# Kernel tuning notes

Measured on AMD Instinct MI355X. Metric: run time of the kernel, lower is better.

The kernel has to match this reference:

```python
import jax, jax.numpy as jnp
import numpy as np

ALPHA = 20.0 / 100.0  # dt / tau
NOISE_SCALE = 0.1 * (2.0 * ALPHA) ** 0.5  # network_noise * sqrt(2*alpha)

T, B, I, H, O = 512, 64, 128, 512, 64


def setup_inputs() -> dict:
    key = jax.random.key(0)
    ks = jax.random.split(key, 6)
    s_in = 1.0 / np.sqrt(I)
    s_h = 1.0 / np.sqrt(H)
    return {
        "x": jax.random.normal(ks[0], (T, B, I), jnp.float32),
        "noise": jax.random.normal(ks[1], (T, B, H), jnp.float32),
        "W_in": jax.random.normal(ks[2], (H, I), jnp.float32) * s_in,
        "W_rec": jax.random.normal(ks[3], (H, H), jnp.float32) * s_h,
        "b_rec": jnp.zeros((H,), jnp.float32),
        "W_out": jax.random.normal(ks[4], (O, H), jnp.float32) * s_h,
        "b_out": jnp.zeros((O,), jnp.float32),
    }


def reference(x, noise, W_in, W_rec, b_rec, W_out, b_out):
    # Precompute input projection for all timesteps: (T, B, H)
    xin = jnp.einsum("tbi,hi->tbh", x, W_in)

    def step(hidden, inp):
        xin_t, noise_t = inp
        h_new = jax.nn.relu(xin_t + hidden @ W_rec.T + b_rec)
        h_new = hidden * (1.0 - ALPHA) + h_new * ALPHA
        h_new = h_new + noise_t * NOISE_SCALE
        return h_new, h_new

    h0 = jnp.zeros((x.shape[1], W_rec.shape[0]), x.dtype)
    _, rnn_output = jax.lax.scan(step, h0, (xin, noise))  # (T, B, H)
    output = jnp.einsum("tbh,oh->tbo", rnn_output, W_out) + b_out
    return output, rnn_output
```

## Files before the change

kernel.cpp:

```cpp
#include <hip/hip_runtime.h>

constexpr int T  = 512;
constexpr int NB = 64;
constexpr int NI = 128;
constexpr int NH = 512;
constexpr int NO = 64;

constexpr float ALPHA = 0.2f;
constexpr float NSC   = 0.063245553203367586f;

typedef _Float16 h2_t __attribute__((ext_vector_type(2)));

#if defined(__has_builtin)
#  if __has_builtin(__builtin_amdgcn_fdot2)
#    define HAS_FDOT2 1
#  endif
#endif
#ifndef HAS_FDOT2
#  define HAS_FDOT2 0
#endif

__device__ __forceinline__ float dot2(uint32_t wbits, uint32_t hbits, float acc) {
#if HAS_FDOT2
    return __builtin_amdgcn_fdot2(__builtin_bit_cast(h2_t, wbits),
                                  __builtin_bit_cast(h2_t, hbits), acc, false);
#else
    const h2_t wv = __builtin_bit_cast(h2_t, wbits);
    const h2_t hv = __builtin_bit_cast(h2_t, hbits);
    return acc + (float)wv.x * (float)hv.x + (float)wv.y * (float)hv.y;
#endif
}

__global__ __launch_bounds__(256) void k_gemm_nt_bias(
    const float* __restrict__ A, const float* __restrict__ Bm,
    const float* __restrict__ bias, float* __restrict__ C,
    int M, int N, int K)
{
    __shared__ __align__(16) float As[32][68];
    __shared__ __align__(16) float Bs[32][68];
    const int tid = threadIdx.x;
    const int tx = tid & 15, ty = tid >> 4;
    const long row0 = (long)blockIdx.x * 64;
    const long col0 = (long)blockIdx.y * 64;
    const int lr = tid >> 3;
    const int lq = tid & 7;

    float acc[4][4] = {};

    for (int kt = 0; kt < K; kt += 32) {
        #pragma unroll
        for (int hh = 0; hh < 2; ++hh) {
            const int r = lr + hh * 32;
            const float4 va = *(const float4*)&A[(size_t)(row0 + r) * K + kt + lq * 4];
            As[lq*4+0][r] = va.x; As[lq*4+1][r] = va.y;
            As[lq*4+2][r] = va.z; As[lq*4+3][r] = va.w;
            const float4 vb = *(const float4*)&Bm[(size_t)(col0 + r) * K + kt + lq * 4];
            Bs[lq*4+0][r] = vb.x; Bs[lq*4+1][r] = vb.y;
            Bs[lq*4+2][r] = vb.z; Bs[lq*4+3][r] = vb.w;
        }
        __syncthreads();
        #pragma unroll
        for (int kk = 0; kk < 32; ++kk) {
            const float4 a4 = *(const float4*)&As[kk][ty * 4];
            const float4 b4 = *(const float4*)&Bs[kk][tx * 4];
            const float a[4] = {a4.x, a4.y, a4.z, a4.w};
            const float b[4] = {b4.x, b4.y, b4.z, b4.w};
            #pragma unroll
            for (int i = 0; i < 4; ++i)
                #pragma unroll
                for (int j = 0; j < 4; ++j)
                    acc[i][j] += a[i] * b[j];
        }
        __syncthreads();
    }

    #pragma unroll
    for (int i = 0; i < 4; ++i) {
        const long r = row0 + ty * 4 + i;
        const int  cc = (int)col0 + tx * 4;
        float4 ov;
        ov.x = acc[i][0] + bias[cc + 0];
        ov.y = acc[i][1] + bias[cc + 1];
        ov.z = acc[i][2] + bias[cc + 2];
        ov.w = acc[i][3] + bias[cc + 3];
        *(float4*)&C[(size_t)r * N + cc] = ov;
    }
}

__device__ __forceinline__ uint32_t pack_h(float h, uint32_t tag) {
    const _Float16 hf = (_Float16)h;
    const uint32_t hb = __builtin_bit_cast(unsigned short, hf);
    return (hb << 16) | (tag & 0xFFFFu);
}

__global__ __launch_bounds__(512, 2) void k_rnn(
    const float* __restrict__ W_rec,
    const float* __restrict__ noise,
    float* __restrict__ rnn,
    uint32_t* __restrict__ ex)
{
    const int bid = blockIdx.x;
    const int g = bid & 63;
    const int m = bid >> 6;
    const int tid = threadIdx.x;
    const int w = tid >> 6;
    const int l = tid & 63;

    __shared__ __align__(16) unsigned short hbf[NH];
    __shared__ __align__(16) float pr[8][128];

    uint32_t wp0[32], wp1[32];
    {
        const float* p0 = W_rec + (size_t)(m * 128 + l) * NH + w * 64;
        const float* p1 = W_rec + (size_t)(m * 128 + l + 64) * NH + w * 64;
        #pragma unroll
        for (int i = 0; i < 16; ++i) {
            const float4 a = *(const float4*)(p0 + i * 4);
            uint32_t u0 = __builtin_bit_cast(uint32_t,
                (h2_t){(_Float16)a.x, (_Float16)a.y});
            uint32_t u1 = __builtin_bit_cast(uint32_t,
                (h2_t){(_Float16)a.z, (_Float16)a.w});
            asm volatile("" : "+v"(u0), "+v"(u1));
            wp0[i * 2] = u0; wp0[i * 2 + 1] = u1;
            const float4 b = *(const float4*)(p1 + i * 4);
            uint32_t v0 = __builtin_bit_cast(uint32_t,
                (h2_t){(_Float16)b.x, (_Float16)b.y});
            uint32_t v1 = __builtin_bit_cast(uint32_t,
                (h2_t){(_Float16)b.z, (_Float16)b.w});
            asm volatile("" : "+v"(v0), "+v"(v1));
            wp1[i * 2] = v0; wp1[i * 2 + 1] = v1;
        }
    }

    const int gc = m * 128 + tid;

    const int q    = tid - 128;
    const int pp   = q >> 7;
    const int pm   = pp + (pp >= m ? 1 : 0);
    const int pcol = pm * 128 + (q & 127);

    hbf[tid] = 0;

    float hreg = 0.f;

    float xin_pf = 0.f, noi_pf = 0.f;
    if (tid < 128) {
        xin_pf = rnn[(size_t)g * NH + gc];
        noi_pf = noise[(size_t)g * NH + gc];
    }
    __syncthreads();

    int alive  = 1;
    int budget = 1 << 16;

    for (int t = 0; t < T; ++t) {
        float aA0 = 0.f, aA1 = 0.f, aB0 = 0.f, aB1 = 0.f;
        {
            const uint4* hp = (const uint4*)&hbf[w * 64];
            #pragma unroll
            for (int i = 0; i < 8; ++i) {
                const uint4 u = hp[i];
                aA0 = dot2(wp0[i*4+0], u.x, aA0);
                aA1 = dot2(wp0[i*4+1], u.y, aA1);
                aA0 = dot2(wp0[i*4+2], u.z, aA0);
                aA1 = dot2(wp0[i*4+3], u.w, aA1);
                aB0 = dot2(wp1[i*4+0], u.x, aB0);
                aB1 = dot2(wp1[i*4+1], u.y, aB1);
                aB0 = dot2(wp1[i*4+2], u.z, aB0);
                aB1 = dot2(wp1[i*4+3], u.w, aB1);
            }
        }
        pr[w][l]      = aA0 + aA1;
        pr[w][l + 64] = aB0 + aB1;
        __syncthreads();

        const uint32_t want = (uint32_t)(t + 1);
        uint32_t* slot = ex + (size_t)(t & 1) * NB * NH;

        if (tid < 128) {
            float sum = 0.f;
            #pragma unroll
            for (int k = 0; k < 8; ++k) sum += pr[k][tid];
            const float hn = fmaxf(xin_pf + sum, 0.f);
            const float nw = (1.f - ALPHA) * hreg + ALPHA * hn + NSC * noi_pf;
            hreg = nw;
            const uint32_t pk = pack_h(nw, want);
            (void)__hip_atomic_exchange(&slot[(size_t)g * NH + gc], pk,
                                        __ATOMIC_RELAXED, __HIP_MEMORY_SCOPE_AGENT);
            hbf[gc] = (unsigned short)(pk >> 16);
            rnn[((size_t)t * NB + g) * NH + gc] = nw;
            const int tn = (t + 1 < T) ? (t + 1) : t;
            xin_pf = rnn[((size_t)tn * NB + g) * NH + gc];
            noi_pf = noise[((size_t)tn * NB + g) * NH + gc];
        } else {
            uint32_t v;
            if (alive) {
                for (;;) {
                    v = __hip_atomic_fetch_or(&slot[(size_t)g * NH + pcol], 0u,
                                              __ATOMIC_RELAXED, __HIP_MEMORY_SCOPE_AGENT);
                    if ((v & 0xFFFFu) == (want & 0xFFFFu)) break;
                    __builtin_amdgcn_s_sleep(1);
                    if (--budget < 0) { alive = 0; break; }
                }
            } else {
                v = __hip_atomic_fetch_or(&slot[(size_t)g * NH + pcol], 0u,
                                          __ATOMIC_RELAXED, __HIP_MEMORY_SCOPE_AGENT);
            }
            hbf[pcol] = (unsigned short)(v >> 16);
        }
        __syncthreads();
    }
}

extern "C" void kernel_launch(void* const* d_in, const int* in_sizes, int n_in,
                              void* d_out, int out_size, void* d_ws, size_t ws_size,
                              hipStream_t stream)
{
    (void)in_sizes; (void)n_in; (void)out_size; (void)ws_size;
    const float* x     = (const float*)d_in[0];
    const float* noise = (const float*)d_in[1];
    const float* W_in  = (const float*)d_in[2];
    const float* W_rec = (const float*)d_in[3];
    const float* b_rec = (const float*)d_in[4];
    const float* W_out = (const float*)d_in[5];
    const float* b_out = (const float*)d_in[6];

    float* out = (float*)d_out;
    float* rnn = out + (size_t)T * NB * NO;

    uint32_t* ex = (uint32_t*)d_ws;

    hipMemsetAsync(ex, 0, (size_t)2 * NB * NH * sizeof(uint32_t), stream);

    hipLaunchKernelGGL(k_gemm_nt_bias, dim3((T * NB) / 64, NH / 64), dim3(256), 0, stream,
                       x, W_in, b_rec, rnn, T * NB, NH, NI);

    hipLaunchKernelGGL(k_rnn, dim3(256), dim3(512), 0, stream,
                       W_rec, noise, rnn, ex);

    hipLaunchKernelGGL(k_gemm_nt_bias, dim3((T * NB) / 64, NO / 64), dim3(256), 0, stream,
                       rnn, W_out, b_out, out, T * NB, NO, NH);
}
```

Before: 732.9 us.

## Stage fp16 recurrent weights in swizzled LDS instead of registers

Each block now converts its 128-row slice of W_rec to fp16 once and stores it in about 128 KB of dynamic shared memory with an XOR swizzle, instead of holding 64 packed weights per thread in VGPRs. Every timestep re-reads the weights from LDS with 16-byte loads alongside the hidden-state reads. The launch-bounds occupancy hint is dropped and the large dynamic LDS size is set explicitly, which limits the CU to one block. The aim is to cut register pressure, but it adds LDS traffic to every serial recurrence step.

```diff
diff --git a/kernel.cpp b/kernel.cpp
--- a/kernel.cpp
+++ b/kernel.cpp
@@ -29,6 +29,10 @@
     const h2_t hv = __builtin_bit_cast(h2_t, hbits);
     return acc + (float)wv.x * (float)hv.x + (float)wv.y * (float)hv.y;
 #endif
+}
+
+__device__ __forceinline__ uint32_t pk2(float x, float y) {
+    return __builtin_bit_cast(uint32_t, (h2_t){(_Float16)x, (_Float16)y});
 }
 
 __global__ __launch_bounds__(256) void k_gemm_nt_bias(
@@ -93,12 +97,17 @@
     return (hb << 16) | (tag & 0xFFFFu);
 }
 
-__global__ __launch_bounds__(512, 2) void k_rnn(
+__global__ __launch_bounds__(512) void k_rnn(
     const float* __restrict__ W_rec,
     const float* __restrict__ noise,
     float* __restrict__ rnn,
     uint32_t* __restrict__ ex)
 {
+    extern __shared__ __align__(16) char smem[];
+    unsigned short* Wl  = (unsigned short*)smem;
+    unsigned short* hbf = (unsigned short*)(smem + 131072);
+    float*          pr  = (float*)(smem + 132096);
+
     const int bid = blockIdx.x;
     const int g = bid & 63;
     const int m = bid >> 6;
@@ -106,29 +115,26 @@
     const int w = tid >> 6;
     const int l = tid & 63;
 
-    __shared__ __align__(16) unsigned short hbf[NH];
-    __shared__ __align__(16) float pr[8][128];
-
-    uint32_t wp0[32], wp1[32];
     {
         const float* p0 = W_rec + (size_t)(m * 128 + l) * NH + w * 64;
         const float* p1 = W_rec + (size_t)(m * 128 + l + 64) * NH + w * 64;
+        const int s = (l & 7) << 4;
+        char* b0 = (char*)Wl + l * 1024 + w * 128 + s;
+        char* b1 = b0 + 65536;
         #pragma unroll
-        for (int i = 0; i < 16; ++i) {
-            const float4 a = *(const float4*)(p0 + i * 4);
-            uint32_t u0 = __builtin_bit_cast(uint32_t,
-                (h2_t){(_Float16)a.x, (_Float16)a.y});
-            uint32_t u1 = __builtin_bit_cast(uint32_t,
-                (h2_t){(_Float16)a.z, (_Float16)a.w});
-            asm volatile("" : "+v"(u0), "+v"(u1));
-            wp0[i * 2] = u0; wp0[i * 2 + 1] = u1;
-            const float4 b = *(const float4*)(p1 + i * 4);
-            uint32_t v0 = __builtin_bit_cast(uint32_t,
-                (h2_t){(_Float16)b.x, (_Float16)b.y});
-            uint32_t v1 = __builtin_bit_cast(uint32_t,
-                (h2_t){(_Float16)b.z, (_Float16)b.w});
-            asm volatile("" : "+v"(v0), "+v"(v1));
-            wp1[i * 2] = v0; wp1[i * 2 + 1] = v1;
+        for (int j = 0; j < 8; ++j) {
+            const float4 qa0 = *(const float4*)(p0 + j * 8);
+            const float4 qa1 = *(const float4*)(p0 + j * 8 + 4);
+            uint4 ca;
+            ca.x = pk2(qa0.x, qa0.y); ca.y = pk2(qa0.z, qa0.w);
+            ca.z = pk2(qa1.x, qa1.y); ca.w = pk2(qa1.z, qa1.w);
+            *(uint4*)((uintptr_t)b0 ^ (unsigned)(j << 4)) = ca;
+            const float4 qb0 = *(const float4*)(p1 + j * 8);
+            const float4 qb1 = *(const float4*)(p1 + j * 8 + 4);
+            uint4 cb;
+            cb.x = pk2(qb0.x, qb0.y); cb.y = pk2(qb0.z, qb0.w);
+            cb.z = pk2(qb1.x, qb1.y); cb.w = pk2(qb1.z, qb1.w);
+            *(uint4*)((uintptr_t)b1 ^ (unsigned)(j << 4)) = cb;
         }
     }
 
@@ -152,26 +158,27 @@
 
     int alive  = 1;
     int budget = 1 << 16;
+
+    const char* wb0 = (const char*)Wl + l * 1024 + w * 128 + ((l & 7) << 4);
+    const char* wb1 = wb0 + 65536;
 
     for (int t = 0; t < T; ++t) {
         float aA0 = 0.f, aA1 = 0.f, aB0 = 0.f, aB1 = 0.f;
         {
             const uint4* hp = (const uint4*)&hbf[w * 64];
             #pragma unroll
-            for (int i = 0; i < 8; ++i) {
-                const uint4 u = hp[i];
-                aA0 = dot2(wp0[i*4+0], u.x, aA0);
-                aA1 = dot2(wp0[i*4+1], u.y, aA1);
-                aA0 = dot2(wp0[i*4+2], u.z, aA0);
-                aA1 = dot2(wp0[i*4+3], u.w, aA1);
-                aB0 = dot2(wp1[i*4+0], u.x, aB0);
-                aB1 = dot2(wp1[i*4+1], u.y, aB1);
-                aB0 = dot2(wp1[i*4+2], u.z, aB0);
-                aB1 = dot2(wp1[i*4+3], u.w, aB1);
+            for (int j = 0; j < 8; ++j) {
+                const uint4 u = hp[j];
+                const uint4 A = *(const uint4*)((uintptr_t)wb0 ^ (unsigned)(j << 4));
+                const uint4 B = *(const uint4*)((uintptr_t)wb1 ^ (unsigned)(j << 4));
+                aA0 = dot2(A.x, u.x, aA0); aA1 = dot2(A.y, u.y, aA1);
+                aA0 = dot2(A.z, u.z, aA0); aA1 = dot2(A.w, u.w, aA1);
+                aB0 = dot2(B.x, u.x, aB0); aB1 = dot2(B.y, u.y, aB1);
+                aB0 = dot2(B.z, u.z, aB0); aB1 = dot2(B.w, u.w, aB1);
             }
         }
-        pr[w][l]      = aA0 + aA1;
-        pr[w][l + 64] = aB0 + aB1;
+        pr[w * 128 + l]      = aA0 + aA1;
+        pr[w * 128 + l + 64] = aB0 + aB1;
         __syncthreads();
 
         const uint32_t want = (uint32_t)(t + 1);
@@ -180,7 +187,7 @@
         if (tid < 128) {
             float sum = 0.f;
             #pragma unroll
-            for (int k = 0; k < 8; ++k) sum += pr[k][tid];
+            for (int k = 0; k < 8; ++k) sum += pr[k * 128 + tid];
             const float hn = fmaxf(xin_pf + sum, 0.f);
             const float nw = (1.f - ALPHA) * hreg + ALPHA * hn + NSC * noi_pf;
             hreg = nw;
@@ -230,12 +237,17 @@
 
     uint32_t* ex = (uint32_t*)d_ws;
 
+    constexpr int RNN_LDS = 131072 + 1024 + 4096;
+
+    (void)hipFuncSetAttribute((const void*)k_rnn,
+                              hipFuncAttributeMaxDynamicSharedMemorySize, RNN_LDS);
+
     hipMemsetAsync(ex, 0, (size_t)2 * NB * NH * sizeof(uint32_t), stream);
 
     hipLaunchKernelGGL(k_gemm_nt_bias, dim3((T * NB) / 64, NH / 64), dim3(256), 0, stream,
                        x, W_in, b_rec, rnn, T * NB, NH, NI);
 
-    hipLaunchKernelGGL(k_rnn, dim3(256), dim3(512), 0, stream,
+    hipLaunchKernelGGL(k_rnn, dim3(256), dim3(512), RNN_LDS, stream,
                        W_rec, noise, rnn, ex);
 
     hipLaunchKernelGGL(k_gemm_nt_bias, dim3((T * NB) / 64, NO / 64), dim3(256), 0, stream,
```

After: 879.6 us. 20.0% more time.
